# Optimization experiments

Measured on AMD Instinct MI355X. Metric: run time of the kernel, lower is better.

Reference implementation:

```python
import jax, jax.numpy as jnp
import numpy as np

EPS = 1e-7


def setup_inputs() -> dict:
    key = jax.random.key(0)
    k1, k2, k3, k4 = jax.random.split(key, 4)
    N, M = 8192, 8192
    inputs = jax.random.normal(k1, (N, 2), dtype=jnp.float32)
    outputs = jax.random.normal(k2, (N,), dtype=jnp.float32)
    x = jax.random.normal(k3, (M, 2), dtype=jnp.float32)
    # positive per-query bandwidths in [0.5, 1.5)
    bandwidth = 0.5 + jax.random.uniform(k4, (M,), dtype=jnp.float32)
    return {"x": x, "inputs": inputs, "outputs": outputs, "bandwidth": bandwidth}


def reference(x, inputs, outputs, bandwidth):
    # Squared pairwise distances (cdist followed by .pow(2) in the original):
    # d2[n, m] = ||inputs[n] - x[m]||^2, computed via the expansion to avoid
    # materializing an (N, M, 2) intermediate.
    a2 = jnp.sum(inputs * inputs, axis=1)  # (N,)
    b2 = jnp.sum(x * x, axis=1)            # (M,)
    d2 = a2[:, None] + b2[None, :] - 2.0 * (inputs @ x.T)  # (N, M)
    d2 = jnp.maximum(d2, 0.0)

    bw = bandwidth[None, :]  # (1, M), per-query bandwidth
    weights = jnp.exp(-d2 / (2.0 * bw * bw))  # (N, M)
    # Normalization over dim 0 (over the N reference points)
    weights = weights / (jnp.sum(weights, axis=0, keepdims=True) + EPS)
    # weights.T @ outputs -> (M,), Nadaraya-Watson weighted sum
    weighted = weights.T @ outputs  # (M,)
    return weighted
```

## Files before the change

### kernel.cpp

```cpp
#include <hip/hip_runtime.h>

#define EPS 1e-7f
#define LOG2E 1.44269504088896340736f

constexpr int SEGS  = 64;
constexpr int BLOCK = 256;

__global__ __launch_bounds__(BLOCK) void nw_pack(
    const float2* __restrict__ inputs,
    const float*  __restrict__ outputs,
    float4*       __restrict__ packed,
    int N)
{
    int i = blockIdx.x * BLOCK + threadIdx.x;
    if (i < N) {
        float2 p = inputs[i];
        packed[i] = make_float4(p.x, p.y, fmaf(p.x, p.x, p.y * p.y), outputs[i]);
    }
}

__global__ __launch_bounds__(BLOCK) void nw_partial(
    const float4* __restrict__ packed,
    const float2* __restrict__ x,
    const float*  __restrict__ bw,
    float2*       __restrict__ partial,
    int N, int M)
{
    const int j   = blockIdx.x * BLOCK + threadIdx.x;
    const int seg = blockIdx.y;
    const int per = (N + SEGS - 1) / SEGS;
    const int i0  = seg * per;
    const int i1  = min(N, i0 + per);

    float c0 = 0.f, c1 = 0.f, c2 = 0.f, c3 = 0.f;
    if (j < M) {
        float2 xj = x[j];
        float  b  = bw[j];
        float  k  = -LOG2E / (2.0f * b * b);
        c0 = k;
        c1 = -2.0f * k * xj.x;
        c2 = -2.0f * k * xj.y;
        c3 = k * fmaf(xj.x, xj.x, xj.y * xj.y);
    }

    float num0 = 0.f, num1 = 0.f, den0 = 0.f, den1 = 0.f;
    int i = i0;
    #pragma unroll 4
    for (; i + 1 < i1; i += 2) {
        float4 pa = packed[i];
        float4 pb = packed[i + 1];
        float ta = fmaf(c0, pa.z, fmaf(c1, pa.x, fmaf(c2, pa.y, c3)));
        float tb = fmaf(c0, pb.z, fmaf(c1, pb.x, fmaf(c2, pb.y, c3)));
        float wa = __builtin_amdgcn_exp2f(ta);
        float wb = __builtin_amdgcn_exp2f(tb);
        num0 = fmaf(wa, pa.w, num0);
        num1 = fmaf(wb, pb.w, num1);
        den0 += wa;
        den1 += wb;
    }
    if (i < i1) {
        float4 pa = packed[i];
        float ta = fmaf(c0, pa.z, fmaf(c1, pa.x, fmaf(c2, pa.y, c3)));
        float wa = __builtin_amdgcn_exp2f(ta);
        num0 = fmaf(wa, pa.w, num0);
        den0 += wa;
    }

    if (j < M) partial[seg * M + j] = make_float2(num0 + num1, den0 + den1);
}

__global__ __launch_bounds__(BLOCK) void nw_finalize(
    const float2* __restrict__ partial,
    float*        __restrict__ out,
    int M)
{
    const int j = blockIdx.x * BLOCK + threadIdx.x;
    if (j >= M) return;
    float num = 0.f, den = 0.f;
    #pragma unroll
    for (int s = 0; s < SEGS; ++s) {
        float2 p = partial[s * M + j];
        num += p.x;
        den += p.y;
    }
    out[j] = num / (den + EPS);
}

extern "C" void kernel_launch(void* const* d_in, const int* in_sizes, int n_in,
                              void* d_out, int out_size, void* d_ws, size_t ws_size,
                              hipStream_t stream) {
    const float2* x       = (const float2*)d_in[0];
    const float2* inputs  = (const float2*)d_in[1];
    const float*  outputs = (const float*) d_in[2];
    const float*  bwv     = (const float*) d_in[3];
    const int N = in_sizes[2];
    const int M = in_sizes[3];
    float*        out     = (float*)d_out;

    float2* partial = (float2*)d_ws;
    float4* packed  = (float4*)((char*)d_ws + (size_t)SEGS * M * sizeof(float2));

    nw_pack<<<dim3((N + BLOCK - 1) / BLOCK), BLOCK, 0, stream>>>(inputs, outputs, packed, N);

    dim3 grid1((M + BLOCK - 1) / BLOCK, SEGS);
    nw_partial<<<grid1, BLOCK, 0, stream>>>(packed, x, bwv, partial, N, M);

    nw_finalize<<<dim3((M + BLOCK - 1) / BLOCK), BLOCK, 0, stream>>>(partial, out, M);
}
```

Before: 79.39 us.

## Fuse point packing into partial kernel and stage segment points in LDS

Removes the separate pack kernel. Each partial block now loads its segment of reference points, computes the squared norm inline, and stores the result as float4 in shared memory. The inner loop reads broadcast LDS entries instead of global packed data, and out-of-range slots are padded so their weights come out as zero. This saves one launch and the workspace round trip. The LDS buffer is fixed at 128 points, so it silently assumes N/SEGS <= 128.

```diff
diff --git a/kernel.cpp b/kernel.cpp
--- a/kernel.cpp
+++ b/kernel.cpp
@@ -3,36 +3,39 @@
 #define EPS 1e-7f
 #define LOG2E 1.44269504088896340736f
 
+constexpr int BLOCK = 256;
 constexpr int SEGS  = 64;
-constexpr int BLOCK = 256;
 
-__global__ __launch_bounds__(BLOCK) void nw_pack(
+__global__ __launch_bounds__(BLOCK) void nw_partial(
+    const float2* __restrict__ x,
     const float2* __restrict__ inputs,
     const float*  __restrict__ outputs,
-    float4*       __restrict__ packed,
-    int N)
-{
-    int i = blockIdx.x * BLOCK + threadIdx.x;
-    if (i < N) {
-        float2 p = inputs[i];
-        packed[i] = make_float4(p.x, p.y, fmaf(p.x, p.x, p.y * p.y), outputs[i]);
-    }
-}
-
-__global__ __launch_bounds__(BLOCK) void nw_partial(
-    const float4* __restrict__ packed,
-    const float2* __restrict__ x,
     const float*  __restrict__ bw,
     float2*       __restrict__ partial,
     int N, int M)
 {
-    const int j   = blockIdx.x * BLOCK + threadIdx.x;
+    constexpr int PTS = 128;
+    __shared__ float4 pts[PTS];
+
+    const int tid = threadIdx.x;
+    const int jg  = blockIdx.x;
     const int seg = blockIdx.y;
     const int per = (N + SEGS - 1) / SEGS;
     const int i0  = seg * per;
-    const int i1  = min(N, i0 + per);
+    const int cnt = min(per, N - i0);
 
-    float c0 = 0.f, c1 = 0.f, c2 = 0.f, c3 = 0.f;
+    for (int t = tid; t < per; t += BLOCK) {
+        if (t < cnt) {
+            float2 p = inputs[i0 + t];
+            pts[t] = make_float4(p.x, p.y, fmaf(p.x, p.x, p.y * p.y),
+                                 outputs[i0 + t]);
+        } else {
+            pts[t] = make_float4(0.f, 0.f, 3.0e38f, 0.f);
+        }
+    }
+
+    const int j = jg * BLOCK + tid;
+    float c0 = 0.f, c1 = 0.f, c2 = 0.f, c3 = -1.0e38f;
     if (j < M) {
         float2 xj = x[j];
         float  b  = bw[j];
@@ -43,12 +46,13 @@
         c3 = k * fmaf(xj.x, xj.x, xj.y * xj.y);
     }
 
+    __syncthreads();
+
     float num0 = 0.f, num1 = 0.f, den0 = 0.f, den1 = 0.f;
-    int i = i0;
-    #pragma unroll 4
-    for (; i + 1 < i1; i += 2) {
-        float4 pa = packed[i];
-        float4 pb = packed[i + 1];
+    #pragma unroll 8
+    for (int l = 0; l < PTS; l += 2) {
+        float4 pa = pts[l];
+        float4 pb = pts[l + 1];
         float ta = fmaf(c0, pa.z, fmaf(c1, pa.x, fmaf(c2, pa.y, c3)));
         float tb = fmaf(c0, pb.z, fmaf(c1, pb.x, fmaf(c2, pb.y, c3)));
         float wa = __builtin_amdgcn_exp2f(ta);
@@ -58,15 +62,9 @@
         den0 += wa;
         den1 += wb;
     }
-    if (i < i1) {
-        float4 pa = packed[i];
-        float ta = fmaf(c0, pa.z, fmaf(c1, pa.x, fmaf(c2, pa.y, c3)));
-        float wa = __builtin_amdgcn_exp2f(ta);
-        num0 = fmaf(wa, pa.w, num0);
-        den0 += wa;
-    }
 
-    if (j < M) partial[seg * M + j] = make_float2(num0 + num1, den0 + den1);
+    if (j < M) partial[(size_t)seg * M + j] = make_float2(num0 + num1,
+                                                          den0 + den1);
 }
 
 __global__ __launch_bounds__(BLOCK) void nw_finalize(
@@ -77,9 +75,9 @@
     const int j = blockIdx.x * BLOCK + threadIdx.x;
     if (j >= M) return;
     float num = 0.f, den = 0.f;
-    #pragma unroll
+    #pragma unroll 8
     for (int s = 0; s < SEGS; ++s) {
-        float2 p = partial[s * M + j];
+        float2 p = partial[(size_t)s * M + j];
         num += p.x;
         den += p.y;
     }
@@ -96,14 +94,10 @@
     const int N = in_sizes[2];
     const int M = in_sizes[3];
     float*        out     = (float*)d_out;
-
-    float2* partial = (float2*)d_ws;
-    float4* packed  = (float4*)((char*)d_ws + (size_t)SEGS * M * sizeof(float2));
-
-    nw_pack<<<dim3((N + BLOCK - 1) / BLOCK), BLOCK, 0, stream>>>(inputs, outputs, packed, N);
+    float2*       partial = (float2*)d_ws;
 
     dim3 grid1((M + BLOCK - 1) / BLOCK, SEGS);
-    nw_partial<<<grid1, BLOCK, 0, stream>>>(packed, x, bwv, partial, N, M);
+    nw_partial<<<grid1, BLOCK, 0, stream>>>(x, inputs, outputs, bwv, partial, N, M);
 
     nw_finalize<<<dim3((M + BLOCK - 1) / BLOCK), BLOCK, 0, stream>>>(partial, out, M);
 }
```

Measured after the change: 76.35 us. 1.04x faster.
